# Performance work log

Hardware: AMD Instinct MI355X
Metric: run time of the kernel (lower is better)

The kernel has to match this reference:

```python
import jax, jax.numpy as jnp
import numpy as np

JACCARD_THRESH = 0.5
NEG_POS = 3
VAR0, VAR1 = 0.1, 0.2
MAX_POS = 256  # static cap on gathered positives for the metric-learning terms


def point_form(boxes):
    # (cx,cy,w,h) -> (xmin,ymin,xmax,ymax)
    return jnp.concatenate([boxes[:, :2] - boxes[:, 2:] / 2,
                            boxes[:, :2] + boxes[:, 2:] / 2], axis=1)


def jaccard(a, b):
    # a: [O,4], b: [D,4] point form
    lt = jnp.maximum(a[:, None, :2], b[None, :, :2])
    rb = jnp.minimum(a[:, None, 2:], b[None, :, 2:])
    wh = jnp.clip(rb - lt, 0.0)
    inter = wh[..., 0] * wh[..., 1]
    area_a = (a[:, 2] - a[:, 0]) * (a[:, 3] - a[:, 1])
    area_b = (b[:, 2] - b[:, 0]) * (b[:, 3] - b[:, 1])
    return inter / (area_a[:, None] + area_b[None, :] - inter)


def encode(matched, priors):
    g_cxcy = ((matched[:, :2] + matched[:, 2:]) / 2 - priors[:, :2]) / (VAR0 * priors[:, 2:])
    g_wh = jnp.log((matched[:, 2:] - matched[:, :2]) / priors[:, 2:]) / VAR1
    return jnp.concatenate([g_cxcy, g_wh], axis=1)


def match_one(truths, labels, poses, priors):
    # standard SSD match (per image)
    ov = jaccard(truths, point_form(priors))          # [O, D]
    best_prior_idx = jnp.argmax(ov, axis=1)           # [O]
    best_truth_ov = jnp.max(ov, axis=0)               # [D]
    best_truth_idx = jnp.argmax(ov, axis=0)           # [D]
    best_truth_ov = best_truth_ov.at[best_prior_idx].set(2.0)
    best_truth_idx = best_truth_idx.at[best_prior_idx].set(jnp.arange(truths.shape[0]))
    matches = truths[best_truth_idx]                  # [D,4]
    conf = labels[best_truth_idx] + 1                 # background=0
    conf = jnp.where(best_truth_ov < JACCARD_THRESH, 0, conf)
    return encode(matches, priors), conf.astype(jnp.int32), poses[best_truth_idx]


def multibox_loss(loc_data, conf_data, line_data, pose_data, dbox_list, targets):
    B, D, C = conf_data.shape
    truths = targets[:, :, 0:4]
    labels = targets[:, :, 4].astype(jnp.int32)
    poses = targets[:, :, 5:8]
    loc_t, conf_t, pose_t = jax.vmap(match_one, in_axes=(0, 0, 0, None))(
        truths, labels, poses, dbox_list)

    pos = conf_t > 0                                  # [B,D]
    posf = pos.astype(loc_data.dtype)

    # smooth-L1 loc loss over positives (sum reduction)
    d = loc_data - loc_t
    sl1 = jnp.where(jnp.abs(d) < 1.0, 0.5 * d * d, jnp.abs(d) - 0.5)
    loss_l = jnp.sum(sl1 * posf[..., None])

    # pose squared-error over positives
    loss_p = jnp.sum((pose_data - pose_t) ** 2 * posf[..., None])

    # per-anchor cross entropy + hard-negative mining (double-argsort rank trick)
    logp = jax.nn.log_softmax(conf_data, axis=-1)
    ce = -jnp.take_along_axis(logp, conf_t[..., None], axis=-1)[..., 0]  # [B,D]
    ce_mined = jnp.where(pos, 0.0, ce)
    loss_idx = jnp.argsort(-ce_mined, axis=1)
    idx_rank = jnp.argsort(loss_idx, axis=1)
    num_pos = jnp.sum(pos.astype(jnp.int32), axis=1, keepdims=True)
    num_neg = jnp.minimum(num_pos * NEG_POS, D)
    neg = idx_rank < num_neg
    loss_c = jnp.sum(ce * (pos | neg).astype(ce.dtype))

    N = jnp.maximum(jnp.sum(posf), 1.0)
    loss_l = loss_l / N
    loss_c = loss_c / N
    loss_p = loss_p / N

    # ---- metric-learning block on gathered positives (static cap) ----
    pos_flat = pos.reshape(-1)
    order = jnp.argsort(jnp.where(pos_flat, 0, 1))[:MAX_POS]  # stable: row-major positives first
    valid = pos_flat[order]                                   # [K]
    emb = line_data.reshape(-1, line_data.shape[-1])[order]   # [K,32] raw embeddings
    lab = conf_t.reshape(-1)[order]                           # [K]
    qp = pose_t.reshape(-1, 3)[order]                         # [K,3]

    # PairMarginMiner / TripletMarginLoss use L2-normalized LpDistance by default
    nemb = emb / jnp.maximum(jnp.linalg.norm(emb, axis=1, keepdims=True), 1e-12)
    sq = jnp.sum((nemb[:, None, :] - nemb[None, :, :]) ** 2, axis=-1)
    dist = jnp.sqrt(jnp.maximum(sq, 1e-12))                   # [K,K]

    K = emb.shape[0]
    eye = jnp.eye(K, dtype=bool)
    vpair = valid[:, None] & valid[None, :] & ~eye
    same = lab[:, None] == lab[None, :]
    pos_pair = vpair & same & (dist > 0.2)   # mined hard positive pairs
    neg_pair = vpair & ~same & (dist < 0.8)  # mined hard negative pairs
    n_pp = jnp.sum(pos_pair)
    n_np = jnp.sum(neg_pair)

    # pairs -> triplets sharing the anchor; TripletMarginLoss(margin=0.2), AvgNonZero reducer
    trip_mask = pos_pair[:, :, None] & neg_pair[:, None, :]           # [K,K,K]
    trip_loss = jax.nn.relu(dist[:, :, None] - dist[:, None, :] + 0.2)
    nz = trip_mask & (trip_loss > 0)
    loss_t = jnp.sum(jnp.where(nz, trip_loss, 0.0)) / jnp.maximum(jnp.sum(nz), 1)

    # Ldesk over mined positive pairs: raw-embedding sq-dist vs pose sq-dist consistency
    e_sq = jnp.sum((emb[:, None, :] - emb[None, :, :]) ** 2, axis=-1)
    q_sq = jnp.sum((qp[:, None, :] - qp[None, :, :]) ** 2, axis=-1)
    desk_sum = jnp.sum(jnp.where(pos_pair, (e_sq - q_sq) ** 2, 0.0))
    npp = jnp.maximum(n_pp, 1).astype(loc_data.dtype)
    Ldesk = desk_sum / npp + loss_t / jnp.maximum(n_pp + n_np, 1)
    Ldesk = Ldesk / npp / 32.0

    return loss_l, loss_c, loss_p, Ldesk, loss_t


def setup_inputs():
    key = jax.random.key(0)
    ks = jax.random.split(key, 10)
    B, D, C, L, O = 32, 8732, 21, 32, 8
    loc_data = jax.random.normal(ks[0], (B, D, 4)) * 0.1
    conf_data = jax.random.normal(ks[1], (B, D, C))
    line_data = jax.random.normal(ks[2], (B, D, L))
    pose_data = jax.random.normal(ks[3], (B, D, 3))
    # default boxes (cx,cy,w,h) in (0,1)
    cxcy = jax.random.uniform(ks[4], (D, 2), minval=0.05, maxval=0.95)
    wh = jax.random.uniform(ks[5], (D, 2), minval=0.05, maxval=0.4)
    dbox_list = jnp.concatenate([cxcy, wh], axis=1)
    # targets: [xmin,ymin,xmax,ymax,label,pose(3),unused]
    mins = jax.random.uniform(ks[6], (B, O, 2), minval=0.0, maxval=0.6)
    sizes = jax.random.uniform(ks[7], (B, O, 2), minval=0.1, maxval=0.4)
    boxes = jnp.concatenate([mins, mins + sizes], axis=-1)
    labs = jax.random.randint(ks[8], (B, O, 1), 0, C - 1).astype(jnp.float32)
    pz = jax.random.normal(ks[9], (B, O, 3))
    targets = jnp.concatenate([boxes, labs, pz, jnp.zeros((B, O, 1))], axis=-1)
    return dict(loc_data=loc_data, conf_data=conf_data, line_data=line_data,
                pose_data=pose_data, dbox_list=dbox_list, targets=targets)


def reference(loc_data, conf_data, line_data, pose_data, dbox_list, targets):
    return multibox_loss(loc_data, conf_data, line_data, pose_data, dbox_list, targets)
```

## Files before the change

### kernel.cpp

```cpp
#include <hip/hip_runtime.h>
#include <cstdint>

#define B 32
#define D 8732
#define C 21
#define L 32
#define O 8
#define NS 8
#define SLICE 1092
#define NT 1024

struct Ws {
  const float *loc, *conf, *line, *pose, *dbox, *targets;
  float* out;
  unsigned long long* bp;
  int* cnt;
  int* posSlice;
  float* sce;
  double *gLossL, *gLossP, *gCeP;
  double *gCeNeg;
  double *gDesk, *gNpp, *gNnp, *gTripS, *gTripC;
  int* gPc;
  float *emb, *nemb, *qp; int* lab;
};

__device__ inline double waveSumD(double v) {
  #pragma unroll
  for (int s = 32; s > 0; s >>= 1) v += __shfl_down(v, s, 64);
  return v;
}

__device__ inline float iou_one(float tx1, float ty1, float tx2, float ty2, float ta,
                                float px1, float py1, float px2, float py2, float areaB) {
  float lx = fmaxf(tx1, px1), ly = fmaxf(ty1, py1);
  float rx = fminf(tx2, px2), ry = fminf(ty2, py2);
  float iw = fmaxf(rx - lx, 0.f), ih = fmaxf(ry - ly, 0.f);
  float inter = iw * ih;
  return inter / (ta + areaB - inter);
}

__global__ __launch_bounds__(256) void k_bp(Ws p) {
  __shared__ float tb[O][4], ta[O];
  __shared__ unsigned long long wm[4][O];
  int g = blockIdx.x, tid = threadIdx.x;
  int lane = tid & 63, wav = tid >> 6;
  int b = g >> 3, s = g & 7;
  int dBeg = s * SLICE;
  int dEnd = dBeg + SLICE; if (dEnd > D) dEnd = D;
  if (tid < O) {
    const float* tr = p.targets + ((size_t)b * O + tid) * 9;
    tb[tid][0] = tr[0]; tb[tid][1] = tr[1]; tb[tid][2] = tr[2]; tb[tid][3] = tr[3];
    ta[tid] = (tr[2] - tr[0]) * (tr[3] - tr[1]);
  }
  __syncthreads();
  unsigned long long key[O];
  #pragma unroll
  for (int t = 0; t < O; t++) key[t] = 0ull;
  for (int d = dBeg + tid; d < dEnd; d += 256) {
    float4 db = *(const float4*)(p.dbox + (size_t)d * 4);
    float px1 = db.x - 0.5f*db.z, py1 = db.y - 0.5f*db.w;
    float px2 = db.x + 0.5f*db.z, py2 = db.y + 0.5f*db.w;
    float areaB = db.z * db.w;
    #pragma unroll
    for (int t = 0; t < O; t++) {
      float iou = iou_one(tb[t][0], tb[t][1], tb[t][2], tb[t][3], ta[t],
                          px1, py1, px2, py2, areaB);
      unsigned long long kk = ((unsigned long long)__float_as_uint(iou) << 32)
                            | (unsigned long long)(0xFFFFFFFFu - (unsigned)d);
      if (kk > key[t]) key[t] = kk;
    }
  }
  #pragma unroll
  for (int t = 0; t < O; t++) {
    unsigned long long k = key[t];
    #pragma unroll
    for (int sft = 32; sft > 0; sft >>= 1) {
      unsigned long long o = __shfl_down(k, sft, 64);
      if (o > k) k = o;
    }
    if (lane == 0) wm[wav][t] = k;
  }
  __syncthreads();
  if (tid < O) {
    unsigned long long k = wm[0][tid];
    #pragma unroll
    for (int w = 1; w < 4; w++) if (wm[w][tid] > k) k = wm[w][tid];
    atomicMax(&p.bp[b * O + tid], k);
  }
}

__global__ __launch_bounds__(NT) void k_slice(Ws p) {
  __shared__ float tb[O][4], ta[O], tl[O], tp_[O][3];
  __shared__ int bpd[O];
  __shared__ int plist[256];
  __shared__ int wcnt[16], wbase[16];
  __shared__ double wred[16][3];
  __shared__ int run;
  int g = blockIdx.x, tid = threadIdx.x;
  int lane = tid & 63, wav = tid >> 6;
  const unsigned long long lt = (lane == 0) ? 0ull : (~0ull >> (64 - lane));
  int b = g >> 3, s = g & 7;
  int dBeg = s * SLICE;
  int dEnd = dBeg + SLICE; if (dEnd > D) dEnd = D;

  if (tid < O) {
    const float* tr = p.targets + ((size_t)b * O + tid) * 9;
    tb[tid][0] = tr[0]; tb[tid][1] = tr[1]; tb[tid][2] = tr[2]; tb[tid][3] = tr[3];
    ta[tid] = (tr[2] - tr[0]) * (tr[3] - tr[1]);
    tl[tid] = tr[4];
    tp_[tid][0] = tr[5]; tp_[tid][1] = tr[6]; tp_[tid][2] = tr[7];
  }
  if (tid >= 64 && tid < 64 + O) {
    unsigned long long k = p.bp[b * O + (tid - 64)];
    bpd[tid - 64] = (int)(0xFFFFFFFFu - (unsigned)(k & 0xFFFFFFFFull));
  }
  if (tid == 0) run = 0;
  __syncthreads();

  double ll = 0, lp = 0, cp = 0;
  for (int d0 = dBeg; d0 < dEnd; d0 += NT) {
    int d = d0 + tid;
    bool act = d < dEnd;
    int cls = 0, bi = 0;
    if (act) {
      float4 db = *(const float4*)(p.dbox + (size_t)d * 4);
      float px1 = db.x - 0.5f*db.z, py1 = db.y - 0.5f*db.w;
      float px2 = db.x + 0.5f*db.z, py2 = db.y + 0.5f*db.w;
      float areaB = db.z * db.w;
      float bv = -1.0f;
      #pragma unroll
      for (int t = 0; t < O; t++) {
        float iou = iou_one(tb[t][0], tb[t][1], tb[t][2], tb[t][3], ta[t],
                            px1, py1, px2, py2, areaB);
        if (iou > bv) { bv = iou; bi = t; }
      }
      #pragma unroll
      for (int t = O - 1; t >= 0; t--)
        if (bpd[t] == d) { bi = t; bv = 2.0f; break; }
      cls = (bv < 0.5f) ? 0 : ((int)tl[bi] + 1);
      const float* cb = p.conf + ((size_t)b * D + d) * C;
      float x[C];
      #pragma unroll
      for (int c = 0; c < C; c++) x[c] = cb[c];
      float m = x[0];
      #pragma unroll
      for (int c = 1; c < C; c++) m = fmaxf(m, x[c]);
      float sm = 0.f;
      #pragma unroll
      for (int c = 0; c < C; c++) sm += __expf(x[c] - m);
      float xc = x[0];
      #pragma unroll
      for (int c = 1; c < C; c++) xc = (cls == c) ? x[c] : xc;
      float ce = m + __logf(sm) - xc;
      size_t bd = (size_t)b * D + d;
      if (cls > 0) {
        cp += ce;
        p.sce[bd] = 0.f;
        float g0 = ((tb[bi][0] + tb[bi][2]) * 0.5f - db.x) / (0.1f * db.z);
        float g1 = ((tb[bi][1] + tb[bi][3]) * 0.5f - db.y) / (0.1f * db.w);
        float g2 = logf((tb[bi][2] - tb[bi][0]) / db.z) / 0.2f;
        float g3 = logf((tb[bi][3] - tb[bi][1]) / db.w) / 0.2f;
        float4 lo = *(const float4*)(p.loc + bd * 4);
        float dv, a;
        dv = lo.x - g0; a = fabsf(dv); ll += (double)((a < 1.f) ? 0.5f*dv*dv : a - 0.5f);
        dv = lo.y - g1; a = fabsf(dv); ll += (double)((a < 1.f) ? 0.5f*dv*dv : a - 0.5f);
        dv = lo.z - g2; a = fabsf(dv); ll += (double)((a < 1.f) ? 0.5f*dv*dv : a - 0.5f);
        dv = lo.w - g3; a = fabsf(dv); ll += (double)((a < 1.f) ? 0.5f*dv*dv : a - 0.5f);
        const float* po = p.pose + bd * 3;
        #pragma unroll
        for (int q = 0; q < 3; q++) {
          float pd = po[q] - tp_[bi][q];
          lp += (double)pd * (double)pd;
        }
      } else {
        p.sce[bd] = fmaxf(ce, 0.f);
      }
    }
    bool pos = act && (cls > 0);
    unsigned long long mm = __ballot(pos);
    if (lane == 0) wcnt[wav] = __popcll(mm);
    __syncthreads();
    if (tid == 0) {
      int r = run;
      #pragma unroll
      for (int w = 0; w < 16; w++) { wbase[w] = r; r += wcnt[w]; }
      run = r;
    }
    __syncthreads();
    if (pos) {
      int rank = wbase[wav] + __popcll(mm & lt);
      if (rank < 256) plist[rank] = d | (cls << 14) | (bi << 19);
    }
    __syncthreads();
  }
  int tot = run;
  if (tid == 0) p.cnt[g] = tot;
  int stored = (tot < 256) ? tot : 256;
  if (tid < stored) p.posSlice[g * 256 + tid] = plist[tid];
  double a0 = waveSumD(ll), a1 = waveSumD(lp), a2 = waveSumD(cp);
  if (lane == 0) { wred[wav][0] = a0; wred[wav][1] = a1; wred[wav][2] = a2; }
  __syncthreads();
  if (tid == 0) {
    double tll = 0, tlp = 0, tcp = 0;
    #pragma unroll
    for (int w = 0; w < 16; w++) { tll += wred[w][0]; tlp += wred[w][1]; tcp += wred[w][2]; }
    p.gLossL[g] = tll; p.gLossP[g] = tlp; p.gCeP[g] = tcp;
  }
}

__global__ __launch_bounds__(NT) void k_batch(Ws p) {
  __shared__ __align__(16) float sce[D];
  __shared__ int whist[16][256];
  __shared__ int hist[256];
  __shared__ int sc[256];
  __shared__ int p8[NS + 1];
  __shared__ int gbS;
  __shared__ unsigned prefixSh; __shared__ int kkSh;
  __shared__ double wsum[16], wcnt2[16];
  int bb = blockIdx.x, tid = threadIdx.x;
  int lane = tid & 63, wav = tid >> 6;
  if (tid < 256) sc[tid] = p.cnt[tid];
  __syncthreads();
  if (tid == 0) {
    int gb = 0;
    for (int i = 0; i < bb * NS; i++) gb += sc[i];
    gbS = gb;
    int run = 0;
    for (int ss = 0; ss < NS; ss++) { p8[ss] = run; run += sc[bb * NS + ss]; }
    p8[NS] = run;
    if (bb == 0) {
      int totAll = 0;
      for (int i = 0; i < 256; i++) totAll += sc[i];
      *p.gPc = (totAll < 256) ? totAll : 256;
    }
  }
  __syncthreads();
  int gb = gbS, npos = p8[NS];
  int nr = (npos < 256) ? npos : 256;
  if (tid < nr) {
    int r = tid, ss = 0;
    #pragma unroll
    for (int q = 1; q < NS; q++) if (r >= p8[q]) ss = q;
    int idx = r - p8[ss];
    int slot = gb + r;
    if (idx < 256 && slot < 256) {
      int packed = p.posSlice[(bb * NS + ss) * 256 + idx];
      int d   = packed & 0x3FFF;
      int cls = (packed >> 14) & 31;
      int bi  = (packed >> 19) & 7;
      size_t flat = (size_t)bb * D + d;
      const float4* e4 = (const float4*)(p.line + flat * L);
      float4* o4 = (float4*)(p.emb + slot * L);
      float4* n4 = (float4*)(p.nemb + slot * L);
      float4 v[8];
      float nrm2 = 0.f;
      #pragma unroll
      for (int c = 0; c < 8; c++) {
        v[c] = e4[c];
        o4[c] = v[c];
        nrm2 += v[c].x*v[c].x + v[c].y*v[c].y + v[c].z*v[c].z + v[c].w*v[c].w;
      }
      float inv = 1.f / fmaxf(sqrtf(nrm2), 1e-12f);
      #pragma unroll
      for (int c = 0; c < 8; c++) {
        float4 t = v[c];
        t.x *= inv; t.y *= inv; t.z *= inv; t.w *= inv;
        n4[c] = t;
      }
      p.lab[slot] = cls;
      const float* tr = p.targets + ((size_t)bb * O + bi) * 9;
      p.qp[slot * 3 + 0] = tr[5]; p.qp[slot * 3 + 1] = tr[6]; p.qp[slot * 3 + 2] = tr[7];
    }
  }
  const float* ce = p.sce + (size_t)bb * D;
  for (int i = tid; i < D / 4; i += NT)
    ((float4*)sce)[i] = ((const float4*)ce)[i];
  int k = npos * 3; if (k > D) k = D;
  __syncthreads();
  unsigned prefix = 0; int kk = k;
  for (int pass = 0; pass < 4; pass++) {
    int shift = 24 - 8 * pass;
    for (int i = tid; i < 16 * 256; i += NT) ((int*)whist)[i] = 0;
    __syncthreads();
    unsigned himask = (pass == 0) ? 0u : (0xFFFFFFFFu << (shift + 8));
    for (int d = tid; d < D; d += NT) {
      unsigned keyb = __float_as_uint(sce[d]);
      if ((keyb & himask) == (prefix & himask))
        atomicAdd(&whist[wav][(keyb >> shift) & 255], 1);
    }
    __syncthreads();
    if (tid < 256) {
      int h = 0;
      #pragma unroll
      for (int w = 0; w < 16; w++) h += whist[w][tid];
      hist[tid] = h;
    }
    __syncthreads();
    if (tid < 64) {
      int l = tid;
      int h0 = hist[l*4], h1 = hist[l*4+1], h2 = hist[l*4+2], h3 = hist[l*4+3];
      int loc4 = h0 + h1 + h2 + h3;
      int suf = loc4;
      #pragma unroll
      for (int st = 1; st < 64; st <<= 1) {
        int o = __shfl_down(suf, st, 64);
        if (l + st < 64) suf += o;
      }
      int snext = suf - loc4;
      int s3 = snext + h3, s2 = s3 + h2, s1 = s2 + h1, s0 = s1 + h0;
      if (s3 >= kk && snext < kk) { prefixSh = prefix | ((unsigned)(l*4+3) << shift); kkSh = kk - snext; }
      if (s2 >= kk && s3 < kk)    { prefixSh = prefix | ((unsigned)(l*4+2) << shift); kkSh = kk - s3; }
      if (s1 >= kk && s2 < kk)    { prefixSh = prefix | ((unsigned)(l*4+1) << shift); kkSh = kk - s2; }
      if (s0 >= kk && s1 < kk)    { prefixSh = prefix | ((unsigned)(l*4+0) << shift); kkSh = kk - s1; }
    }
    __syncthreads();
    prefix = prefixSh; kk = kkSh;
    __syncthreads();
  }
  float T = __uint_as_float(prefix);
  double sgt = 0.0; int cgt = 0;
  for (int d = tid; d < D; d += NT) {
    float v = sce[d];
    if (__float_as_uint(v) > prefix) { sgt += (double)v; cgt++; }
  }
  double wv = waveSumD(sgt);
  double wc = waveSumD((double)cgt);
  if (lane == 0) { wsum[wav] = wv; wcnt2[wav] = wc; }
  __syncthreads();
  if (tid == 0) {
    double tsg = 0, tcg = 0;
    #pragma unroll
    for (int w = 0; w < 16; w++) { tsg += wsum[w]; tcg += wcnt2[w]; }
    p.gCeNeg[bb] = tsg + ((double)k - tcg) * (double)T;
  }
}

__global__ __launch_bounds__(NT) void k_pt2(Ws p) {
  __shared__ float ei[L], ni[L], qi[3];
  __shared__ float sd[256];
  __shared__ unsigned long long spm[4], snm[4];
  __shared__ double w1[4];
  __shared__ int ppc[4], npc[4];
  __shared__ double wS[16], wC[16];
  __shared__ int liS, pcS;
  int i = blockIdx.x, tid = threadIdx.x;
  int lane = tid & 63, wav = tid >> 6;
  int qq = tid >> 8, j = tid & 255;
  if (tid == 0) { pcS = *p.gPc; liS = p.lab[i]; }
  if (tid < L) { ei[tid] = p.emb[i * L + tid]; ni[tid] = p.nemb[i * L + tid]; }
  if (tid >= L && tid < L + 3) qi[tid - L] = p.qp[i * 3 + (tid - L)];
  __syncthreads();
  int Pc = pcS, li = liS;
  bool vi = (i < Pc);
  bool pp = false, np = false;
  double dsk = 0.0;
  if (qq == 0) {
    bool vj = (j < Pc);
    const float4* nj4 = (const float4*)(p.nemb + j * L);
    const float4* ej4 = (const float4*)(p.emb + j * L);
    float sq = 0.f, esq = 0.f;
    #pragma unroll
    for (int c = 0; c < 8; c++) {
      float4 nn = nj4[c], ee = ej4[c];
      float d0 = ni[c*4+0] - nn.x, d1 = ni[c*4+1] - nn.y;
      float d2 = ni[c*4+2] - nn.z, d3 = ni[c*4+3] - nn.w;
      sq += d0*d0 + d1*d1 + d2*d2 + d3*d3;
      float e0 = ei[c*4+0] - ee.x, e1 = ei[c*4+1] - ee.y;
      float e2 = ei[c*4+2] - ee.z, e3 = ei[c*4+3] - ee.w;
      esq += e0*e0 + e1*e1 + e2*e2 + e3*e3;
    }
    float dd = sqrtf(fmaxf(sq, 1e-12f));
    sd[j] = dd;
    float qsq = 0.f;
    #pragma unroll
    for (int c = 0; c < 3; c++) { float dq = qi[c] - p.qp[j * 3 + c]; qsq += dq * dq; }
    bool vp = vi && vj && (i != j);
    bool same = (li == p.lab[j]);
    pp = vp && same && (dd > 0.2f);
    np = vp && !same && (dd < 0.8f);
    float diff = esq - qsq;
    dsk = pp ? (double)diff * (double)diff : 0.0;
  }
  unsigned long long pb = __ballot(pp), nb = __ballot(np);
  double dw = waveSumD(dsk);
  if (lane == 0 && wav < 4) {
    spm[wav] = pb; snm[wav] = nb; w1[wav] = dw;
    ppc[wav] = (int)__popcll(pb); npc[wav] = (int)__popcll(nb);
  }
  __syncthreads();
  unsigned long long pmw = spm[j >> 6];
  bool pj = (pmw >> (j & 63)) & 1ull;
  float sdj = sd[j];
  double ts = 0.0, tc = 0.0;
  if (pj) {
    for (int it = 0; it < 64; it++) {
      int kx = qq + 4 * it;
      unsigned long long nmw = snm[kx >> 6];
      if ((nmw >> (kx & 63)) & 1ull) {
        float x = sdj - sd[kx] + 0.2f;
        if (x > 0.f) { ts += (double)x; tc += 1.0; }
      }
    }
  }
  ts = waveSumD(ts); tc = waveSumD(tc);
  if (lane == 0) { wS[wav] = ts; wC[wav] = tc; }
  __syncthreads();
  if (tid == 0) {
    double S = 0, Cc = 0;
    #pragma unroll
    for (int w = 0; w < 16; w++) { S += wS[w]; Cc += wC[w]; }
    double dsum = w1[0] + w1[1] + w1[2] + w1[3];
    int pcnt = ppc[0] + ppc[1] + ppc[2] + ppc[3];
    int ncnt = npc[0] + npc[1] + npc[2] + npc[3];
    p.gDesk[i] = dsum; p.gNpp[i] = (double)pcnt; p.gNnp[i] = (double)ncnt;
    p.gTripS[i] = S; p.gTripC[i] = Cc;
  }
}

__global__ __launch_bounds__(256) void k_fin(Ws p) {
  __shared__ double lbuf[4];
  int tid = threadIdx.x;
  auto sumD = [&](const double* a, int n) -> double {
    double v = 0;
    for (int i = tid; i < n; i += 256) v += a[i];
    v = waveSumD(v);
    __syncthreads();
    if ((tid & 63) == 0) lbuf[tid >> 6] = v;
    __syncthreads();
    double r = lbuf[0] + lbuf[1] + lbuf[2] + lbuf[3];
    __syncthreads();
    return r;
  };
  double lossL = sumD(p.gLossL, 256);
  double lossP = sumD(p.gLossP, 256);
  double ceP   = sumD(p.gCeP,   256);
  double ceN   = sumD(p.gCeNeg,  B);
  double desk  = sumD(p.gDesk,  256);
  double npp   = sumD(p.gNpp,   256);
  double nnp   = sumD(p.gNnp,   256);
  double tripS = sumD(p.gTripS, 256);
  double tripC = sumD(p.gTripC, 256);
  double Ntot;
  {
    double v = 0;
    for (int i = tid; i < 256; i += 256) v += (double)p.cnt[i];
    v = waveSumD(v);
    __syncthreads();
    if ((tid & 63) == 0) lbuf[tid >> 6] = v;
    __syncthreads();
    Ntot = lbuf[0] + lbuf[1] + lbuf[2] + lbuf[3];
  }
  if (tid == 0) {
    double N = (Ntot > 0.0) ? Ntot : 1.0;
    p.out[0] = (float)(lossL / N);
    p.out[1] = (float)((ceP + ceN) / N);
    p.out[2] = (float)(lossP / N);
    double cnt = (tripC > 0.0) ? tripC : 1.0;
    double loss_t = tripS / cnt;
    double nppd = (npp > 0.0) ? npp : 1.0;
    double tot = npp + nnp;
    double denom = (tot > 0.0) ? tot : 1.0;
    double Ldesk = desk / nppd + loss_t / denom;
    Ldesk = Ldesk / nppd / 32.0;
    p.out[3] = (float)Ldesk;
    p.out[4] = (float)loss_t;
  }
}

extern "C" void kernel_launch(void* const* d_in, const int* in_sizes, int n_in,
                              void* d_out, int out_size, void* d_ws, size_t ws_size,
                              hipStream_t stream) {
  char* ws = (char*)d_ws;
  size_t off = 0;
  auto alloc = [&](size_t bytes) -> char* {
    char* q = ws + off;
    off += (bytes + 255) & ~(size_t)255;
    return q;
  };
  Ws p;
  p.loc     = (const float*)d_in[0];
  p.conf    = (const float*)d_in[1];
  p.line    = (const float*)d_in[2];
  p.pose    = (const float*)d_in[3];
  p.dbox    = (const float*)d_in[4];
  p.targets = (const float*)d_in[5];
  p.out     = (float*)d_out;
  p.bp       = (unsigned long long*)alloc(B * O * 8);
  p.cnt      = (int*)alloc(256 * 4);
  p.posSlice = (int*)alloc(256 * 256 * 4);
  p.sce      = (float*)alloc((size_t)B * D * 4);
  p.gLossL   = (double*)alloc(256 * 8);
  p.gLossP   = (double*)alloc(256 * 8);
  p.gCeP     = (double*)alloc(256 * 8);
  p.gCeNeg   = (double*)alloc(B * 8);
  p.gDesk    = (double*)alloc(256 * 8);
  p.gNpp     = (double*)alloc(256 * 8);
  p.gNnp     = (double*)alloc(256 * 8);
  p.gTripS   = (double*)alloc(256 * 8);
  p.gTripC   = (double*)alloc(256 * 8);
  p.gPc      = (int*)alloc(256);
  p.emb      = (float*)alloc(256 * L * 4);
  p.nemb     = (float*)alloc(256 * L * 4);
  p.qp       = (float*)alloc(256 * 3 * 4);
  p.lab      = (int*)alloc(256 * 4);

  hipMemsetAsync(p.bp, 0, B * O * 8, stream);
  k_bp   <<<256, 256, 0, stream>>>(p);
  k_slice<<<256, NT, 0, stream>>>(p);
  k_batch<<<B,   NT, 0, stream>>>(p);
  k_pt2  <<<256, NT, 0, stream>>>(p);
  k_fin  <<<1,  256, 0, stream>>>(p);
}
```

Measured before the change: 155.0 us.

## Fuse five kernels into one cooperative persistent kernel with grid syncs

Merges the best-prior, slice, batch, pairwise and final-reduction kernels into a single cooperative kernel that separates its phases with grid.sync(), and overlays their shared memory in a union. The best-prior step now writes per-block partial keys instead of using atomicMax, which also removes the memset. The intent is to cut the launch and inter-kernel gap overhead of a chain of small kernels. In exchange, it depends on all 256 blocks of 1024 threads being co-resident, and the grid barriers can cost more than the gaps they replace. The union makes every phase carry the largest shared-memory footprint, which may limit occupancy.

```diff
diff --git a/kernel.cpp b/kernel.cpp
--- a/kernel.cpp
+++ b/kernel.cpp
@@ -1,5 +1,8 @@
 #include <hip/hip_runtime.h>
+#include <hip/hip_cooperative_groups.h>
 #include <cstdint>
+
+namespace cg = cooperative_groups;
 
 #define B 32
 #define D 8732
@@ -39,431 +42,444 @@
   return inter / (ta + areaB - inter);
 }
 
-__global__ __launch_bounds__(256) void k_bp(Ws p) {
-  __shared__ float tb[O][4], ta[O];
-  __shared__ unsigned long long wm[4][O];
+struct ShA {
+  float tb[O][4], ta[O], tl[O], tp_[O][3];
+  unsigned long long wm[16][O];
+  int bpd[O];
+  int plist[256];
+  int wcnt[16], wbase[16];
+  double wred[16][3];
+  int run;
+};
+struct __align__(16) ShB {
+  float sce[D];
+  int whist[16][256];
+  int hist[256];
+  int sc[256];
+  int p8[NS + 1];
+  int gbS;
+  unsigned prefixSh; int kkSh;
+  double wsum[16], wcnt2[16];
+};
+struct ShC {
+  float ei[L], ni[L], qi[3];
+  float sd[256];
+  unsigned long long spm[4], snm[4];
+  double w1[4];
+  int ppc[4], npc[4];
+  double wS[16], wC[16];
+  int liS, pcS;
+};
+struct ShD { double lbuf[16]; };
+union ShU { ShA a; ShB b; ShC c; ShD d; };
+
+__global__ __launch_bounds__(NT, 4) void k_all(Ws p) {
+  __shared__ ShU sh;
+  cg::grid_group grid = cg::this_grid();
   int g = blockIdx.x, tid = threadIdx.x;
   int lane = tid & 63, wav = tid >> 6;
   int b = g >> 3, s = g & 7;
   int dBeg = s * SLICE;
   int dEnd = dBeg + SLICE; if (dEnd > D) dEnd = D;
+
   if (tid < O) {
     const float* tr = p.targets + ((size_t)b * O + tid) * 9;
-    tb[tid][0] = tr[0]; tb[tid][1] = tr[1]; tb[tid][2] = tr[2]; tb[tid][3] = tr[3];
-    ta[tid] = (tr[2] - tr[0]) * (tr[3] - tr[1]);
+    sh.a.tb[tid][0] = tr[0]; sh.a.tb[tid][1] = tr[1];
+    sh.a.tb[tid][2] = tr[2]; sh.a.tb[tid][3] = tr[3];
+    sh.a.ta[tid] = (tr[2] - tr[0]) * (tr[3] - tr[1]);
+    sh.a.tl[tid] = tr[4];
+    sh.a.tp_[tid][0] = tr[5]; sh.a.tp_[tid][1] = tr[6]; sh.a.tp_[tid][2] = tr[7];
   }
   __syncthreads();
-  unsigned long long key[O];
-  #pragma unroll
-  for (int t = 0; t < O; t++) key[t] = 0ull;
-  for (int d = dBeg + tid; d < dEnd; d += 256) {
-    float4 db = *(const float4*)(p.dbox + (size_t)d * 4);
-    float px1 = db.x - 0.5f*db.z, py1 = db.y - 0.5f*db.w;
-    float px2 = db.x + 0.5f*db.z, py2 = db.y + 0.5f*db.w;
-    float areaB = db.z * db.w;
+
+  {
+    unsigned long long key[O];
     #pragma unroll
-    for (int t = 0; t < O; t++) {
-      float iou = iou_one(tb[t][0], tb[t][1], tb[t][2], tb[t][3], ta[t],
-                          px1, py1, px2, py2, areaB);
-      unsigned long long kk = ((unsigned long long)__float_as_uint(iou) << 32)
-                            | (unsigned long long)(0xFFFFFFFFu - (unsigned)d);
-      if (kk > key[t]) key[t] = kk;
-    }
-  }
-  #pragma unroll
-  for (int t = 0; t < O; t++) {
-    unsigned long long k = key[t];
-    #pragma unroll
-    for (int sft = 32; sft > 0; sft >>= 1) {
-      unsigned long long o = __shfl_down(k, sft, 64);
-      if (o > k) k = o;
-    }
-    if (lane == 0) wm[wav][t] = k;
-  }
-  __syncthreads();
-  if (tid < O) {
-    unsigned long long k = wm[0][tid];
-    #pragma unroll
-    for (int w = 1; w < 4; w++) if (wm[w][tid] > k) k = wm[w][tid];
-    atomicMax(&p.bp[b * O + tid], k);
-  }
-}
-
-__global__ __launch_bounds__(NT) void k_slice(Ws p) {
-  __shared__ float tb[O][4], ta[O], tl[O], tp_[O][3];
-  __shared__ int bpd[O];
-  __shared__ int plist[256];
-  __shared__ int wcnt[16], wbase[16];
-  __shared__ double wred[16][3];
-  __shared__ int run;
-  int g = blockIdx.x, tid = threadIdx.x;
-  int lane = tid & 63, wav = tid >> 6;
-  const unsigned long long lt = (lane == 0) ? 0ull : (~0ull >> (64 - lane));
-  int b = g >> 3, s = g & 7;
-  int dBeg = s * SLICE;
-  int dEnd = dBeg + SLICE; if (dEnd > D) dEnd = D;
-
-  if (tid < O) {
-    const float* tr = p.targets + ((size_t)b * O + tid) * 9;
-    tb[tid][0] = tr[0]; tb[tid][1] = tr[1]; tb[tid][2] = tr[2]; tb[tid][3] = tr[3];
-    ta[tid] = (tr[2] - tr[0]) * (tr[3] - tr[1]);
-    tl[tid] = tr[4];
-    tp_[tid][0] = tr[5]; tp_[tid][1] = tr[6]; tp_[tid][2] = tr[7];
-  }
-  if (tid >= 64 && tid < 64 + O) {
-    unsigned long long k = p.bp[b * O + (tid - 64)];
-    bpd[tid - 64] = (int)(0xFFFFFFFFu - (unsigned)(k & 0xFFFFFFFFull));
-  }
-  if (tid == 0) run = 0;
-  __syncthreads();
-
-  double ll = 0, lp = 0, cp = 0;
-  for (int d0 = dBeg; d0 < dEnd; d0 += NT) {
-    int d = d0 + tid;
-    bool act = d < dEnd;
-    int cls = 0, bi = 0;
-    if (act) {
+    for (int t = 0; t < O; t++) key[t] = 0ull;
+    for (int d = dBeg + tid; d < dEnd; d += NT) {
       float4 db = *(const float4*)(p.dbox + (size_t)d * 4);
       float px1 = db.x - 0.5f*db.z, py1 = db.y - 0.5f*db.w;
       float px2 = db.x + 0.5f*db.z, py2 = db.y + 0.5f*db.w;
       float areaB = db.z * db.w;
-      float bv = -1.0f;
       #pragma unroll
       for (int t = 0; t < O; t++) {
-        float iou = iou_one(tb[t][0], tb[t][1], tb[t][2], tb[t][3], ta[t],
-                            px1, py1, px2, py2, areaB);
-        if (iou > bv) { bv = iou; bi = t; }
-      }
-      #pragma unroll
-      for (int t = O - 1; t >= 0; t--)
-        if (bpd[t] == d) { bi = t; bv = 2.0f; break; }
-      cls = (bv < 0.5f) ? 0 : ((int)tl[bi] + 1);
-      const float* cb = p.conf + ((size_t)b * D + d) * C;
-      float x[C];
-      #pragma unroll
-      for (int c = 0; c < C; c++) x[c] = cb[c];
-      float m = x[0];
-      #pragma unroll
-      for (int c = 1; c < C; c++) m = fmaxf(m, x[c]);
-      float sm = 0.f;
-      #pragma unroll
-      for (int c = 0; c < C; c++) sm += __expf(x[c] - m);
-      float xc = x[0];
-      #pragma unroll
-      for (int c = 1; c < C; c++) xc = (cls == c) ? x[c] : xc;
-      float ce = m + __logf(sm) - xc;
-      size_t bd = (size_t)b * D + d;
-      if (cls > 0) {
-        cp += ce;
-        p.sce[bd] = 0.f;
-        float g0 = ((tb[bi][0] + tb[bi][2]) * 0.5f - db.x) / (0.1f * db.z);
-        float g1 = ((tb[bi][1] + tb[bi][3]) * 0.5f - db.y) / (0.1f * db.w);
-        float g2 = logf((tb[bi][2] - tb[bi][0]) / db.z) / 0.2f;
-        float g3 = logf((tb[bi][3] - tb[bi][1]) / db.w) / 0.2f;
-        float4 lo = *(const float4*)(p.loc + bd * 4);
-        float dv, a;
-        dv = lo.x - g0; a = fabsf(dv); ll += (double)((a < 1.f) ? 0.5f*dv*dv : a - 0.5f);
-        dv = lo.y - g1; a = fabsf(dv); ll += (double)((a < 1.f) ? 0.5f*dv*dv : a - 0.5f);
-        dv = lo.z - g2; a = fabsf(dv); ll += (double)((a < 1.f) ? 0.5f*dv*dv : a - 0.5f);
-        dv = lo.w - g3; a = fabsf(dv); ll += (double)((a < 1.f) ? 0.5f*dv*dv : a - 0.5f);
-        const float* po = p.pose + bd * 3;
-        #pragma unroll
-        for (int q = 0; q < 3; q++) {
-          float pd = po[q] - tp_[bi][q];
-          lp += (double)pd * (double)pd;
+        float iou = iou_one(sh.a.tb[t][0], sh.a.tb[t][1], sh.a.tb[t][2], sh.a.tb[t][3],
+                            sh.a.ta[t], px1, py1, px2, py2, areaB);
+        unsigned long long kk = ((unsigned long long)__float_as_uint(iou) << 32)
+                              | (unsigned long long)(0xFFFFFFFFu - (unsigned)d);
+        if (kk > key[t]) key[t] = kk;
+      }
+    }
+    #pragma unroll
+    for (int t = 0; t < O; t++) {
+      unsigned long long k = key[t];
+      #pragma unroll
+      for (int sft = 32; sft > 0; sft >>= 1) {
+        unsigned long long o = __shfl_down(k, sft, 64);
+        if (o > k) k = o;
+      }
+      if (lane == 0) sh.a.wm[wav][t] = k;
+    }
+    __syncthreads();
+    if (tid < O) {
+      unsigned long long k = sh.a.wm[0][tid];
+      #pragma unroll
+      for (int w = 1; w < 16; w++) if (sh.a.wm[w][tid] > k) k = sh.a.wm[w][tid];
+      p.bp[g * O + tid] = k;
+    }
+  }
+  grid.sync();
+
+  {
+    if (tid < O) {
+      unsigned long long k = 0ull;
+      #pragma unroll
+      for (int ss = 0; ss < NS; ss++) {
+        unsigned long long kk = p.bp[(b * NS + ss) * O + tid];
+        if (kk > k) k = kk;
+      }
+      sh.a.bpd[tid] = (int)(0xFFFFFFFFu - (unsigned)(k & 0xFFFFFFFFull));
+    }
+    if (tid == 0) sh.a.run = 0;
+    __syncthreads();
+
+    const unsigned long long lt = (lane == 0) ? 0ull : (~0ull >> (64 - lane));
+    double ll = 0, lp = 0, cp = 0;
+    for (int d0 = dBeg; d0 < dEnd; d0 += NT) {
+      int d = d0 + tid;
+      bool act = d < dEnd;
+      int cls = 0, bi = 0;
+      if (act) {
+        float4 db = *(const float4*)(p.dbox + (size_t)d * 4);
+        float px1 = db.x - 0.5f*db.z, py1 = db.y - 0.5f*db.w;
+        float px2 = db.x + 0.5f*db.z, py2 = db.y + 0.5f*db.w;
+        float areaB = db.z * db.w;
+        float bv = -1.0f;
+        #pragma unroll
+        for (int t = 0; t < O; t++) {
+          float iou = iou_one(sh.a.tb[t][0], sh.a.tb[t][1], sh.a.tb[t][2], sh.a.tb[t][3],
+                              sh.a.ta[t], px1, py1, px2, py2, areaB);
+          if (iou > bv) { bv = iou; bi = t; }
         }
-      } else {
-        p.sce[bd] = fmaxf(ce, 0.f);
-      }
-    }
-    bool pos = act && (cls > 0);
-    unsigned long long mm = __ballot(pos);
-    if (lane == 0) wcnt[wav] = __popcll(mm);
+        #pragma unroll
+        for (int t = O - 1; t >= 0; t--)
+          if (sh.a.bpd[t] == d) { bi = t; bv = 2.0f; break; }
+        cls = (bv < 0.5f) ? 0 : ((int)sh.a.tl[bi] + 1);
+        const float* cb = p.conf + ((size_t)b * D + d) * C;
+        float x[C];
+        #pragma unroll
+        for (int c = 0; c < C; c++) x[c] = cb[c];
+        float m = x[0];
+        #pragma unroll
+        for (int c = 1; c < C; c++) m = fmaxf(m, x[c]);
+        float sm = 0.f;
+        #pragma unroll
+        for (int c = 0; c < C; c++) sm += __expf(x[c] - m);
+        float xc = x[0];
+        #pragma unroll
+        for (int c = 1; c < C; c++) xc = (cls == c) ? x[c] : xc;
+        float ce = m + __logf(sm) - xc;
+        size_t bd = (size_t)b * D + d;
+        if (cls > 0) {
+          cp += ce;
+          p.sce[bd] = 0.f;
+          float g0 = ((sh.a.tb[bi][0] + sh.a.tb[bi][2]) * 0.5f - db.x) / (0.1f * db.z);
+          float g1 = ((sh.a.tb[bi][1] + sh.a.tb[bi][3]) * 0.5f - db.y) / (0.1f * db.w);
+          float g2 = logf((sh.a.tb[bi][2] - sh.a.tb[bi][0]) / db.z) / 0.2f;
+          float g3 = logf((sh.a.tb[bi][3] - sh.a.tb[bi][1]) / db.w) / 0.2f;
+          float4 lo = *(const float4*)(p.loc + bd * 4);
+          float dv, a;
+          dv = lo.x - g0; a = fabsf(dv); ll += (double)((a < 1.f) ? 0.5f*dv*dv : a - 0.5f);
+          dv = lo.y - g1; a = fabsf(dv); ll += (double)((a < 1.f) ? 0.5f*dv*dv : a - 0.5f);
+          dv = lo.z - g2; a = fabsf(dv); ll += (double)((a < 1.f) ? 0.5f*dv*dv : a - 0.5f);
+          dv = lo.w - g3; a = fabsf(dv); ll += (double)((a < 1.f) ? 0.5f*dv*dv : a - 0.5f);
+          const float* po = p.pose + bd * 3;
+          #pragma unroll
+          for (int q = 0; q < 3; q++) {
+            float pd = po[q] - sh.a.tp_[bi][q];
+            lp += (double)pd * (double)pd;
+          }
+        } else {
+          p.sce[bd] = fmaxf(ce, 0.f);
+        }
+      }
+      bool pos = act && (cls > 0);
+      unsigned long long mm = __ballot(pos);
+      if (lane == 0) sh.a.wcnt[wav] = __popcll(mm);
+      __syncthreads();
+      if (tid == 0) {
+        int r = sh.a.run;
+        #pragma unroll
+        for (int w = 0; w < 16; w++) { sh.a.wbase[w] = r; r += sh.a.wcnt[w]; }
+        sh.a.run = r;
+      }
+      __syncthreads();
+      if (pos) {
+        int rank = sh.a.wbase[wav] + __popcll(mm & lt);
+        if (rank < 256) sh.a.plist[rank] = d | (cls << 14) | (bi << 19);
+      }
+      __syncthreads();
+    }
+    int tot = sh.a.run;
+    if (tid == 0) p.cnt[g] = tot;
+    int stored = (tot < 256) ? tot : 256;
+    if (tid < stored) p.posSlice[g * 256 + tid] = sh.a.plist[tid];
+    double a0 = waveSumD(ll), a1 = waveSumD(lp), a2 = waveSumD(cp);
+    if (lane == 0) { sh.a.wred[wav][0] = a0; sh.a.wred[wav][1] = a1; sh.a.wred[wav][2] = a2; }
     __syncthreads();
     if (tid == 0) {
-      int r = run;
-      #pragma unroll
-      for (int w = 0; w < 16; w++) { wbase[w] = r; r += wcnt[w]; }
-      run = r;
-    }
-    __syncthreads();
-    if (pos) {
-      int rank = wbase[wav] + __popcll(mm & lt);
-      if (rank < 256) plist[rank] = d | (cls << 14) | (bi << 19);
-    }
-    __syncthreads();
+      double tll = 0, tlp = 0, tcp = 0;
+      #pragma unroll
+      for (int w = 0; w < 16; w++) { tll += sh.a.wred[w][0]; tlp += sh.a.wred[w][1]; tcp += sh.a.wred[w][2]; }
+      p.gLossL[g] = tll; p.gLossP[g] = tlp; p.gCeP[g] = tcp;
+    }
   }
-  int tot = run;
-  if (tid == 0) p.cnt[g] = tot;
-  int stored = (tot < 256) ? tot : 256;
-  if (tid < stored) p.posSlice[g * 256 + tid] = plist[tid];
-  double a0 = waveSumD(ll), a1 = waveSumD(lp), a2 = waveSumD(cp);
-  if (lane == 0) { wred[wav][0] = a0; wred[wav][1] = a1; wred[wav][2] = a2; }
-  __syncthreads();
-  if (tid == 0) {
-    double tll = 0, tlp = 0, tcp = 0;
-    #pragma unroll
-    for (int w = 0; w < 16; w++) { tll += wred[w][0]; tlp += wred[w][1]; tcp += wred[w][2]; }
-    p.gLossL[g] = tll; p.gLossP[g] = tlp; p.gCeP[g] = tcp;
+  grid.sync();
+
+  if (g < B) {
+    int bb = g;
+    if (tid < 256) sh.b.sc[tid] = p.cnt[tid];
+    __syncthreads();
+    if (tid == 0) {
+      int gb2 = 0;
+      for (int i = 0; i < bb * NS; i++) gb2 += sh.b.sc[i];
+      sh.b.gbS = gb2;
+      int run2 = 0;
+      for (int ss = 0; ss < NS; ss++) { sh.b.p8[ss] = run2; run2 += sh.b.sc[bb * NS + ss]; }
+      sh.b.p8[NS] = run2;
+      if (bb == 0) {
+        int totAll = 0;
+        for (int i = 0; i < 256; i++) totAll += sh.b.sc[i];
+        *p.gPc = (totAll < 256) ? totAll : 256;
+      }
+    }
+    __syncthreads();
+    int gb = sh.b.gbS, npos = sh.b.p8[NS];
+    int nr = (npos < 256) ? npos : 256;
+    if (tid < nr) {
+      int r = tid, ss = 0;
+      #pragma unroll
+      for (int q = 1; q < NS; q++) if (r >= sh.b.p8[q]) ss = q;
+      int idx = r - sh.b.p8[ss];
+      int slot = gb + r;
+      if (idx < 256 && slot < 256) {
+        int packed = p.posSlice[(bb * NS + ss) * 256 + idx];
+        int d   = packed & 0x3FFF;
+        int cls = (packed >> 14) & 31;
+        int bi  = (packed >> 19) & 7;
+        size_t flat = (size_t)bb * D + d;
+        const float4* e4 = (const float4*)(p.line + flat * L);
+        float4* o4 = (float4*)(p.emb + slot * L);
+        float4* n4 = (float4*)(p.nemb + slot * L);
+        float4 v[8];
+        float nrm2 = 0.f;
+        #pragma unroll
+        for (int c = 0; c < 8; c++) {
+          v[c] = e4[c];
+          o4[c] = v[c];
+          nrm2 += v[c].x*v[c].x + v[c].y*v[c].y + v[c].z*v[c].z + v[c].w*v[c].w;
+        }
+        float inv = 1.f / fmaxf(sqrtf(nrm2), 1e-12f);
+        #pragma unroll
+        for (int c = 0; c < 8; c++) {
+          float4 t = v[c];
+          t.x *= inv; t.y *= inv; t.z *= inv; t.w *= inv;
+          n4[c] = t;
+        }
+        p.lab[slot] = cls;
+        const float* tr = p.targets + ((size_t)bb * O + bi) * 9;
+        p.qp[slot * 3 + 0] = tr[5]; p.qp[slot * 3 + 1] = tr[6]; p.qp[slot * 3 + 2] = tr[7];
+      }
+    }
+    const float* ce = p.sce + (size_t)bb * D;
+    for (int i = tid; i < D / 4; i += NT)
+      ((float4*)sh.b.sce)[i] = ((const float4*)ce)[i];
+    int k = npos * 3; if (k > D) k = D;
+    __syncthreads();
+    unsigned prefix = 0; int kk = k;
+    for (int pass = 0; pass < 4; pass++) {
+      int shift = 24 - 8 * pass;
+      for (int i = tid; i < 16 * 256; i += NT) ((int*)sh.b.whist)[i] = 0;
+      __syncthreads();
+      unsigned himask = (pass == 0) ? 0u : (0xFFFFFFFFu << (shift + 8));
+      for (int d = tid; d < D; d += NT) {
+        unsigned keyb = __float_as_uint(sh.b.sce[d]);
+        if ((keyb & himask) == (prefix & himask))
+          atomicAdd(&sh.b.whist[wav][(keyb >> shift) & 255], 1);
+      }
+      __syncthreads();
+      if (tid < 256) {
+        int h = 0;
+        #pragma unroll
+        for (int w = 0; w < 16; w++) h += sh.b.whist[w][tid];
+        sh.b.hist[tid] = h;
+      }
+      __syncthreads();
+      if (tid < 64) {
+        int l = tid;
+        int h0 = sh.b.hist[l*4], h1 = sh.b.hist[l*4+1], h2 = sh.b.hist[l*4+2], h3 = sh.b.hist[l*4+3];
+        int loc4 = h0 + h1 + h2 + h3;
+        int suf = loc4;
+        #pragma unroll
+        for (int st = 1; st < 64; st <<= 1) {
+          int o = __shfl_down(suf, st, 64);
+          if (l + st < 64) suf += o;
+        }
+        int snext = suf - loc4;
+        int s3 = snext + h3, s2 = s3 + h2, s1 = s2 + h1, s0 = s1 + h0;
+        if (s3 >= kk && snext < kk) { sh.b.prefixSh = prefix | ((unsigned)(l*4+3) << shift); sh.b.kkSh = kk - snext; }
+        if (s2 >= kk && s3 < kk)    { sh.b.prefixSh = prefix | ((unsigned)(l*4+2) << shift); sh.b.kkSh = kk - s3; }
+        if (s1 >= kk && s2 < kk)    { sh.b.prefixSh = prefix | ((unsigned)(l*4+1) << shift); sh.b.kkSh = kk - s2; }
+        if (s0 >= kk && s1 < kk)    { sh.b.prefixSh = prefix | ((unsigned)(l*4+0) << shift); sh.b.kkSh = kk - s1; }
+      }
+      __syncthreads();
+      prefix = sh.b.prefixSh; kk = sh.b.kkSh;
+      __syncthreads();
+    }
+    float T = __uint_as_float(prefix);
+    double sgt = 0.0; int cgt = 0;
+    for (int d = tid; d < D; d += NT) {
+      float v = sh.b.sce[d];
+      if (__float_as_uint(v) > prefix) { sgt += (double)v; cgt++; }
+    }
+    double wv = waveSumD(sgt);
+    double wc = waveSumD((double)cgt);
+    if (lane == 0) { sh.b.wsum[wav] = wv; sh.b.wcnt2[wav] = wc; }
+    __syncthreads();
+    if (tid == 0) {
+      double tsg = 0, tcg = 0;
+      #pragma unroll
+      for (int w = 0; w < 16; w++) { tsg += sh.b.wsum[w]; tcg += sh.b.wcnt2[w]; }
+      p.gCeNeg[bb] = tsg + ((double)k - tcg) * (double)T;
+    }
   }
-}
-
-__global__ __launch_bounds__(NT) void k_batch(Ws p) {
-  __shared__ __align__(16) float sce[D];
-  __shared__ int whist[16][256];
-  __shared__ int hist[256];
-  __shared__ int sc[256];
-  __shared__ int p8[NS + 1];
-  __shared__ int gbS;
-  __shared__ unsigned prefixSh; __shared__ int kkSh;
-  __shared__ double wsum[16], wcnt2[16];
-  int bb = blockIdx.x, tid = threadIdx.x;
-  int lane = tid & 63, wav = tid >> 6;
-  if (tid < 256) sc[tid] = p.cnt[tid];
-  __syncthreads();
-  if (tid == 0) {
-    int gb = 0;
-    for (int i = 0; i < bb * NS; i++) gb += sc[i];
-    gbS = gb;
-    int run = 0;
-    for (int ss = 0; ss < NS; ss++) { p8[ss] = run; run += sc[bb * NS + ss]; }
-    p8[NS] = run;
-    if (bb == 0) {
-      int totAll = 0;
-      for (int i = 0; i < 256; i++) totAll += sc[i];
-      *p.gPc = (totAll < 256) ? totAll : 256;
+  grid.sync();
+
+  {
+    int i = g;
+    int qq = tid >> 8, j = tid & 255;
+    if (tid == 0) { sh.c.pcS = *p.gPc; sh.c.liS = p.lab[i]; }
+    if (tid < L) { sh.c.ei[tid] = p.emb[i * L + tid]; sh.c.ni[tid] = p.nemb[i * L + tid]; }
+    if (tid >= L && tid < L + 3) sh.c.qi[tid - L] = p.qp[i * 3 + (tid - L)];
+    __syncthreads();
+    int Pc = sh.c.pcS, li = sh.c.liS;
+    bool vi = (i < Pc);
+    bool pp = false, np = false;
+    double dsk = 0.0;
+    if (qq == 0) {
+      bool vj = (j < Pc);
+      const float4* nj4 = (const float4*)(p.nemb + j * L);
+      const float4* ej4 = (const float4*)(p.emb + j * L);
+      float sq = 0.f, esq = 0.f;
+      #pragma unroll
+      for (int c = 0; c < 8; c++) {
+        float4 nn = nj4[c], ee = ej4[c];
+        float d0 = sh.c.ni[c*4+0] - nn.x, d1 = sh.c.ni[c*4+1] - nn.y;
+        float d2 = sh.c.ni[c*4+2] - nn.z, d3 = sh.c.ni[c*4+3] - nn.w;
+        sq += d0*d0 + d1*d1 + d2*d2 + d3*d3;
+        float e0 = sh.c.ei[c*4+0] - ee.x, e1 = sh.c.ei[c*4+1] - ee.y;
+        float e2 = sh.c.ei[c*4+2] - ee.z, e3 = sh.c.ei[c*4+3] - ee.w;
+        esq += e0*e0 + e1*e1 + e2*e2 + e3*e3;
+      }
+      float dd = sqrtf(fmaxf(sq, 1e-12f));
+      sh.c.sd[j] = dd;
+      float qsq = 0.f;
+      #pragma unroll
+      for (int c = 0; c < 3; c++) { float dq = sh.c.qi[c] - p.qp[j * 3 + c]; qsq += dq * dq; }
+      bool vp = vi && vj && (i != j);
+      bool same = (li == p.lab[j]);
+      pp = vp && same && (dd > 0.2f);
+      np = vp && !same && (dd < 0.8f);
+      float diff = esq - qsq;
+      dsk = pp ? (double)diff * (double)diff : 0.0;
+    }
+    unsigned long long pb = __ballot(pp), nb = __ballot(np);
+    double dw = waveSumD(dsk);
+    if (lane == 0 && wav < 4) {
+      sh.c.spm[wav] = pb; sh.c.snm[wav] = nb; sh.c.w1[wav] = dw;
+      sh.c.ppc[wav] = (int)__popcll(pb); sh.c.npc[wav] = (int)__popcll(nb);
+    }
+    __syncthreads();
+    unsigned long long pmw = sh.c.spm[j >> 6];
+    bool pj = (pmw >> (j & 63)) & 1ull;
+    float sdj = sh.c.sd[j];
+    double ts = 0.0, tc = 0.0;
+    if (pj) {
+      for (int it = 0; it < 64; it++) {
+        int kx = qq + 4 * it;
+        unsigned long long nmw = sh.c.snm[kx >> 6];
+        if ((nmw >> (kx & 63)) & 1ull) {
+          float x = sdj - sh.c.sd[kx] + 0.2f;
+          if (x > 0.f) { ts += (double)x; tc += 1.0; }
+        }
+      }
+    }
+    ts = waveSumD(ts); tc = waveSumD(tc);
+    if (lane == 0) { sh.c.wS[wav] = ts; sh.c.wC[wav] = tc; }
+    __syncthreads();
+    if (tid == 0) {
+      double S = 0, Cc = 0;
+      #pragma unroll
+      for (int w = 0; w < 16; w++) { S += sh.c.wS[w]; Cc += sh.c.wC[w]; }
+      double dsum = sh.c.w1[0] + sh.c.w1[1] + sh.c.w1[2] + sh.c.w1[3];
+      int pcnt = sh.c.ppc[0] + sh.c.ppc[1] + sh.c.ppc[2] + sh.c.ppc[3];
+      int ncnt = sh.c.npc[0] + sh.c.npc[1] + sh.c.npc[2] + sh.c.npc[3];
+      p.gDesk[i] = dsum; p.gNpp[i] = (double)pcnt; p.gNnp[i] = (double)ncnt;
+      p.gTripS[i] = S; p.gTripC[i] = Cc;
     }
   }
-  __syncthreads();
-  int gb = gbS, npos = p8[NS];
-  int nr = (npos < 256) ? npos : 256;
-  if (tid < nr) {
-    int r = tid, ss = 0;
-    #pragma unroll
-    for (int q = 1; q < NS; q++) if (r >= p8[q]) ss = q;
-    int idx = r - p8[ss];
-    int slot = gb + r;
-    if (idx < 256 && slot < 256) {
-      int packed = p.posSlice[(bb * NS + ss) * 256 + idx];
-      int d   = packed & 0x3FFF;
-      int cls = (packed >> 14) & 31;
-      int bi  = (packed >> 19) & 7;
-      size_t flat = (size_t)bb * D + d;
-      const float4* e4 = (const float4*)(p.line + flat * L);
-      float4* o4 = (float4*)(p.emb + slot * L);
-      float4* n4 = (float4*)(p.nemb + slot * L);
-      float4 v[8];
-      float nrm2 = 0.f;
-      #pragma unroll
-      for (int c = 0; c < 8; c++) {
-        v[c] = e4[c];
-        o4[c] = v[c];
-        nrm2 += v[c].x*v[c].x + v[c].y*v[c].y + v[c].z*v[c].z + v[c].w*v[c].w;
-      }
-      float inv = 1.f / fmaxf(sqrtf(nrm2), 1e-12f);
-      #pragma unroll
-      for (int c = 0; c < 8; c++) {
-        float4 t = v[c];
-        t.x *= inv; t.y *= inv; t.z *= inv; t.w *= inv;
-        n4[c] = t;
-      }
-      p.lab[slot] = cls;
-      const float* tr = p.targets + ((size_t)bb * O + bi) * 9;
-      p.qp[slot * 3 + 0] = tr[5]; p.qp[slot * 3 + 1] = tr[6]; p.qp[slot * 3 + 2] = tr[7];
-    }
-  }
-  const float* ce = p.sce + (size_t)bb * D;
-  for (int i = tid; i < D / 4; i += NT)
-    ((float4*)sce)[i] = ((const float4*)ce)[i];
-  int k = npos * 3; if (k > D) k = D;
-  __syncthreads();
-  unsigned prefix = 0; int kk = k;
-  for (int pass = 0; pass < 4; pass++) {
-    int shift = 24 - 8 * pass;
-    for (int i = tid; i < 16 * 256; i += NT) ((int*)whist)[i] = 0;
-    __syncthreads();
-    unsigned himask = (pass == 0) ? 0u : (0xFFFFFFFFu << (shift + 8));
-    for (int d = tid; d < D; d += NT) {
-      unsigned keyb = __float_as_uint(sce[d]);
-      if ((keyb & himask) == (prefix & himask))
-        atomicAdd(&whist[wav][(keyb >> shift) & 255], 1);
-    }
-    __syncthreads();
-    if (tid < 256) {
-      int h = 0;
-      #pragma unroll
-      for (int w = 0; w < 16; w++) h += whist[w][tid];
-      hist[tid] = h;
-    }
-    __syncthreads();
-    if (tid < 64) {
-      int l = tid;
-      int h0 = hist[l*4], h1 = hist[l*4+1], h2 = hist[l*4+2], h3 = hist[l*4+3];
-      int loc4 = h0 + h1 + h2 + h3;
-      int suf = loc4;
-      #pragma unroll
-      for (int st = 1; st < 64; st <<= 1) {
-        int o = __shfl_down(suf, st, 64);
-        if (l + st < 64) suf += o;
-      }
-      int snext = suf - loc4;
-      int s3 = snext + h3, s2 = s3 + h2, s1 = s2 + h1, s0 = s1 + h0;
-      if (s3 >= kk && snext < kk) { prefixSh = prefix | ((unsigned)(l*4+3) << shift); kkSh = kk - snext; }
-      if (s2 >= kk && s3 < kk)    { prefixSh = prefix | ((unsigned)(l*4+2) << shift); kkSh = kk - s3; }
-      if (s1 >= kk && s2 < kk)    { prefixSh = prefix | ((unsigned)(l*4+1) << shift); kkSh = kk - s2; }
-      if (s0 >= kk && s1 < kk)    { prefixSh = prefix | ((unsigned)(l*4+0) << shift); kkSh = kk - s1; }
-    }
-    __syncthreads();
-    prefix = prefixSh; kk = kkSh;
-    __syncthreads();
-  }
-  float T = __uint_as_float(prefix);
-  double sgt = 0.0; int cgt = 0;
-  for (int d = tid; d < D; d += NT) {
-    float v = sce[d];
-    if (__float_as_uint(v) > prefix) { sgt += (double)v; cgt++; }
-  }
-  double wv = waveSumD(sgt);
-  double wc = waveSumD((double)cgt);
-  if (lane == 0) { wsum[wav] = wv; wcnt2[wav] = wc; }
-  __syncthreads();
-  if (tid == 0) {
-    double tsg = 0, tcg = 0;
-    #pragma unroll
-    for (int w = 0; w < 16; w++) { tsg += wsum[w]; tcg += wcnt2[w]; }
-    p.gCeNeg[bb] = tsg + ((double)k - tcg) * (double)T;
-  }
-}
-
-__global__ __launch_bounds__(NT) void k_pt2(Ws p) {
-  __shared__ float ei[L], ni[L], qi[3];
-  __shared__ float sd[256];
-  __shared__ unsigned long long spm[4], snm[4];
-  __shared__ double w1[4];
-  __shared__ int ppc[4], npc[4];
-  __shared__ double wS[16], wC[16];
-  __shared__ int liS, pcS;
-  int i = blockIdx.x, tid = threadIdx.x;
-  int lane = tid & 63, wav = tid >> 6;
-  int qq = tid >> 8, j = tid & 255;
-  if (tid == 0) { pcS = *p.gPc; liS = p.lab[i]; }
-  if (tid < L) { ei[tid] = p.emb[i * L + tid]; ni[tid] = p.nemb[i * L + tid]; }
-  if (tid >= L && tid < L + 3) qi[tid - L] = p.qp[i * 3 + (tid - L)];
-  __syncthreads();
-  int Pc = pcS, li = liS;
-  bool vi = (i < Pc);
-  bool pp = false, np = false;
-  double dsk = 0.0;
-  if (qq == 0) {
-    bool vj = (j < Pc);
-    const float4* nj4 = (const float4*)(p.nemb + j * L);
-    const float4* ej4 = (const float4*)(p.emb + j * L);
-    float sq = 0.f, esq = 0.f;
-    #pragma unroll
-    for (int c = 0; c < 8; c++) {
-      float4 nn = nj4[c], ee = ej4[c];
-      float d0 = ni[c*4+0] - nn.x, d1 = ni[c*4+1] - nn.y;
-      float d2 = ni[c*4+2] - nn.z, d3 = ni[c*4+3] - nn.w;
-      sq += d0*d0 + d1*d1 + d2*d2 + d3*d3;
-      float e0 = ei[c*4+0] - ee.x, e1 = ei[c*4+1] - ee.y;
-      float e2 = ei[c*4+2] - ee.z, e3 = ei[c*4+3] - ee.w;
-      esq += e0*e0 + e1*e1 + e2*e2 + e3*e3;
-    }
-    float dd = sqrtf(fmaxf(sq, 1e-12f));
-    sd[j] = dd;
-    float qsq = 0.f;
-    #pragma unroll
-    for (int c = 0; c < 3; c++) { float dq = qi[c] - p.qp[j * 3 + c]; qsq += dq * dq; }
-    bool vp = vi && vj && (i != j);
-    bool same = (li == p.lab[j]);
-    pp = vp && same && (dd > 0.2f);
-    np = vp && !same && (dd < 0.8f);
-    float diff = esq - qsq;
-    dsk = pp ? (double)diff * (double)diff : 0.0;
-  }
-  unsigned long long pb = __ballot(pp), nb = __ballot(np);
-  double dw = waveSumD(dsk);
-  if (lane == 0 && wav < 4) {
-    spm[wav] = pb; snm[wav] = nb; w1[wav] = dw;
-    ppc[wav] = (int)__popcll(pb); npc[wav] = (int)__popcll(nb);
-  }
-  __syncthreads();
-  unsigned long long pmw = spm[j >> 6];
-  bool pj = (pmw >> (j & 63)) & 1ull;
-  float sdj = sd[j];
-  double ts = 0.0, tc = 0.0;
-  if (pj) {
-    for (int it = 0; it < 64; it++) {
-      int kx = qq + 4 * it;
-      unsigned long long nmw = snm[kx >> 6];
-      if ((nmw >> (kx & 63)) & 1ull) {
-        float x = sdj - sd[kx] + 0.2f;
-        if (x > 0.f) { ts += (double)x; tc += 1.0; }
-      }
-    }
-  }
-  ts = waveSumD(ts); tc = waveSumD(tc);
-  if (lane == 0) { wS[wav] = ts; wC[wav] = tc; }
-  __syncthreads();
-  if (tid == 0) {
-    double S = 0, Cc = 0;
-    #pragma unroll
-    for (int w = 0; w < 16; w++) { S += wS[w]; Cc += wC[w]; }
-    double dsum = w1[0] + w1[1] + w1[2] + w1[3];
-    int pcnt = ppc[0] + ppc[1] + ppc[2] + ppc[3];
-    int ncnt = npc[0] + npc[1] + npc[2] + npc[3];
-    p.gDesk[i] = dsum; p.gNpp[i] = (double)pcnt; p.gNnp[i] = (double)ncnt;
-    p.gTripS[i] = S; p.gTripC[i] = Cc;
-  }
-}
-
-__global__ __launch_bounds__(256) void k_fin(Ws p) {
-  __shared__ double lbuf[4];
-  int tid = threadIdx.x;
-  auto sumD = [&](const double* a, int n) -> double {
-    double v = 0;
-    for (int i = tid; i < n; i += 256) v += a[i];
-    v = waveSumD(v);
-    __syncthreads();
-    if ((tid & 63) == 0) lbuf[tid >> 6] = v;
-    __syncthreads();
-    double r = lbuf[0] + lbuf[1] + lbuf[2] + lbuf[3];
-    __syncthreads();
-    return r;
-  };
-  double lossL = sumD(p.gLossL, 256);
-  double lossP = sumD(p.gLossP, 256);
-  double ceP   = sumD(p.gCeP,   256);
-  double ceN   = sumD(p.gCeNeg,  B);
-  double desk  = sumD(p.gDesk,  256);
-  double npp   = sumD(p.gNpp,   256);
-  double nnp   = sumD(p.gNnp,   256);
-  double tripS = sumD(p.gTripS, 256);
-  double tripC = sumD(p.gTripC, 256);
-  double Ntot;
-  {
-    double v = 0;
-    for (int i = tid; i < 256; i += 256) v += (double)p.cnt[i];
-    v = waveSumD(v);
-    __syncthreads();
-    if ((tid & 63) == 0) lbuf[tid >> 6] = v;
-    __syncthreads();
-    Ntot = lbuf[0] + lbuf[1] + lbuf[2] + lbuf[3];
-  }
-  if (tid == 0) {
-    double N = (Ntot > 0.0) ? Ntot : 1.0;
-    p.out[0] = (float)(lossL / N);
-    p.out[1] = (float)((ceP + ceN) / N);
-    p.out[2] = (float)(lossP / N);
-    double cnt = (tripC > 0.0) ? tripC : 1.0;
-    double loss_t = tripS / cnt;
-    double nppd = (npp > 0.0) ? npp : 1.0;
-    double tot = npp + nnp;
-    double denom = (tot > 0.0) ? tot : 1.0;
-    double Ldesk = desk / nppd + loss_t / denom;
-    Ldesk = Ldesk / nppd / 32.0;
-    p.out[3] = (float)Ldesk;
-    p.out[4] = (float)loss_t;
+  grid.sync();
+
+  if (g == 0) {
+    auto sumD = [&](const double* a, int n) -> double {
+      double v = 0;
+      for (int i = tid; i < n; i += NT) v += a[i];
+      v = waveSumD(v);
+      __syncthreads();
+      if (lane == 0) sh.d.lbuf[wav] = v;
+      __syncthreads();
+      double r = 0;
+      #pragma unroll
+      for (int w = 0; w < 16; w++) r += sh.d.lbuf[w];
+      __syncthreads();
+      return r;
+    };
+    double lossL = sumD(p.gLossL, 256);
+    double lossP = sumD(p.gLossP, 256);
+    double ceP   = sumD(p.gCeP,   256);
+    double ceN   = sumD(p.gCeNeg,  B);
+    double desk  = sumD(p.gDesk,  256);
+    double npp   = sumD(p.gNpp,   256);
+    double nnp   = sumD(p.gNnp,   256);
+    double tripS = sumD(p.gTripS, 256);
+    double tripC = sumD(p.gTripC, 256);
+    double Ntot;
+    {
+      double v = 0;
+      for (int i = tid; i < 256; i += NT) v += (double)p.cnt[i];
+      v = waveSumD(v);
+      __syncthreads();
+      if (lane == 0) sh.d.lbuf[wav] = v;
+      __syncthreads();
+      Ntot = 0;
+      #pragma unroll
+      for (int w = 0; w < 16; w++) Ntot += sh.d.lbuf[w];
+    }
+    if (tid == 0) {
+      double N = (Ntot > 0.0) ? Ntot : 1.0;
+      p.out[0] = (float)(lossL / N);
+      p.out[1] = (float)((ceP + ceN) / N);
+      p.out[2] = (float)(lossP / N);
+      double cnt = (tripC > 0.0) ? tripC : 1.0;
+      double loss_t = tripS / cnt;
+      double nppd = (npp > 0.0) ? npp : 1.0;
+      double tot = npp + nnp;
+      double denom = (tot > 0.0) ? tot : 1.0;
+      double Ldesk = desk / nppd + loss_t / denom;
+      Ldesk = Ldesk / nppd / 32.0;
+      p.out[3] = (float)Ldesk;
+      p.out[4] = (float)loss_t;
+    }
   }
 }
 
@@ -485,7 +501,7 @@
   p.dbox    = (const float*)d_in[4];
   p.targets = (const float*)d_in[5];
   p.out     = (float*)d_out;
-  p.bp       = (unsigned long long*)alloc(B * O * 8);
+  p.bp       = (unsigned long long*)alloc(256 * O * 8);
   p.cnt      = (int*)alloc(256 * 4);
   p.posSlice = (int*)alloc(256 * 256 * 4);
   p.sce      = (float*)alloc((size_t)B * D * 4);
@@ -504,10 +520,6 @@
   p.qp       = (float*)alloc(256 * 3 * 4);
   p.lab      = (int*)alloc(256 * 4);
 
-  hipMemsetAsync(p.bp, 0, B * O * 8, stream);
-  k_bp   <<<256, 256, 0, stream>>>(p);
-  k_slice<<<256, NT, 0, stream>>>(p);
-  k_batch<<<B,   NT, 0, stream>>>(p);
-  k_pt2  <<<256, NT, 0, stream>>>(p);
-  k_fin  <<<1,  256, 0, stream>>>(p);
+  void* args[] = { (void*)&p };
+  hipLaunchCooperativeKernel((void*)k_all, dim3(256), dim3(NT), args, 0, stream);
 }
```

Result: slower. 303.5 us (+95.8%).
